# Performance work log

Hardware: AMD Instinct MI355X
Metric: run time of the kernel (lower is better)

The kernel has to match this reference:

```python
import jax, jax.numpy as jnp
import numpy as np

B, N, M, H, NH = 128, 4096, 64, 512, 4
IN, OUT = 256, 256
NH2 = 2 * NH  # read/write heads interleaved: even idx = read, odd idx = write
EPS = 1e-8


def setup_inputs() -> dict:
    key = jax.random.key(0)
    ks = jax.random.split(key, 20)
    nrm = lambda k, shape, s=0.05: (jax.random.normal(k, shape, jnp.float32) * s)
    return {
        'in_data': jax.random.normal(ks[0], (B, IN), jnp.float32),
        'memory': jax.random.normal(ks[1], (B, N, M), jnp.float32) * 0.1,
        'h_prev': jax.random.normal(ks[2], (B, H), jnp.float32),
        'c_prev': jax.random.normal(ks[3], (B, H), jnp.float32),
        'prev_reads': jax.random.normal(ks[4], (NH, B, M), jnp.float32),
        'prev_weights': jax.random.uniform(ks[5], (NH2, B, N), jnp.float32),
        # controller LSTMCell (input = in_data ++ prev_reads)
        'W_ih': nrm(ks[6], (4 * H, IN + NH * M)),
        'b_ih': jnp.zeros((4 * H,), jnp.float32),
        'W_hh': nrm(ks[7], (4 * H, H)),
        'b_hh': jnp.zeros((4 * H,), jnp.float32),
        # output layer over [h ++ reads]
        'W_out': nrm(ks[8], (OUT, H + NH * M)),
        'b_out': jnp.zeros((OUT,), jnp.float32),
        # per-head addressing params, stacked over the 2*NH heads (fed with c-state)
        'Wk': nrm(ks[9], (NH2, M, H)), 'bk': jnp.zeros((NH2, M), jnp.float32),
        'Wbeta': nrm(ks[10], (NH2, H)), 'bbeta': jnp.zeros((NH2,), jnp.float32),
        'Wg': nrm(ks[11], (NH2, H)), 'bg': jnp.zeros((NH2,), jnp.float32),
        'Ws': nrm(ks[12], (NH2, 3, H)), 'bs': jnp.zeros((NH2, 3), jnp.float32),
        'Wgam': nrm(ks[13], (NH2, H)), 'bgam': jnp.zeros((NH2,), jnp.float32),
        'We': nrm(ks[14], (NH2, M, H)), 'be': jnp.zeros((NH2, M), jnp.float32),
        'Wa': nrm(ks[15], (NH2, M, H)), 'ba': jnp.zeros((NH2, M), jnp.float32),
    }


def reference(in_data, memory, h_prev, c_prev, prev_reads, prev_weights,
              W_ih, b_ih, W_hh, b_hh, W_out, b_out,
              Wk, bk, Wbeta, bbeta, Wg, bg, Ws, bs, Wgam, bgam, We, be, Wa, ba):
    bsz = in_data.shape[0]
    # controller LSTM step on [x ++ prev_reads]
    x = jnp.concatenate([in_data, jnp.swapaxes(prev_reads, 0, 1).reshape(bsz, -1)], axis=-1)
    gates = x @ W_ih.T + h_prev @ W_hh.T + b_ih + b_hh
    gi, gf, gg, go = jnp.split(gates, 4, axis=-1)
    c = jax.nn.sigmoid(gf) * c_prev + jax.nn.sigmoid(gi) * jnp.tanh(gg)
    h = jax.nn.sigmoid(go) * jnp.tanh(c)  # |h| < 1, so clamp(-20, 20) is identity

    mem = memory
    reads = []
    for i in range(NH2):  # fixed small loop; even = read head, odd = write head
        keyv = c @ Wk[i].T + bk[i]                                    # [B, M]
        beta = jax.nn.softplus(c @ Wbeta[i] + bbeta[i])[:, None]      # [B, 1]
        g = jax.nn.sigmoid(c @ Wg[i] + bg[i])[:, None]                # [B, 1]
        s = jax.nn.softmax(c @ Ws[i].T + bs[i], axis=-1)              # [B, 3]
        gamma = 1.0 + jax.nn.softplus(c @ Wgam[i] + bgam[i])[:, None]  # [B, 1]
        # content addressing: cosine similarity, sharpened softmax
        sim = jnp.einsum('bnm,bm->bn', mem, keyv)
        sim = sim / (jnp.linalg.norm(mem, axis=-1) * jnp.linalg.norm(keyv, axis=-1, keepdims=True) + EPS)
        wc = jax.nn.softmax(beta * sim, axis=-1)
        # interpolate, circular shift (-1, 0, +1), sharpen
        wg_ = g * wc + (1.0 - g) * prev_weights[i]
        wsft = (s[:, 0:1] * jnp.roll(wg_, -1, axis=1)
                + s[:, 1:2] * wg_
                + s[:, 2:3] * jnp.roll(wg_, 1, axis=1))
        wpow = wsft ** gamma
        w = wpow / (jnp.sum(wpow, axis=1, keepdims=True) + EPS)
        if i % 2 == 0:
            reads.append(jnp.einsum('bn,bnm->bm', w, mem))
        else:
            e = jax.nn.sigmoid(c @ We[i].T + be[i])                   # erase [B, M]
            a = jnp.tanh(c @ Wa[i].T + ba[i])                         # add   [B, M]
            mem = mem * (1.0 - w[:, :, None] * e[:, None, :]) + w[:, :, None] * a[:, None, :]

    out = jax.nn.sigmoid(jnp.concatenate([h] + reads, axis=-1) @ W_out.T + b_out)
    return out
```

## Files before the change

kernel.cpp:

```cpp
#include <hip/hip_runtime.h>
#include <math.h>

#define BSZ 128
#define NN_ 4096
#define MM_ 64
#define HH_ 512
#define EPSF 1e-8f

__device__ __forceinline__ float sigmoidf_(float x) { return 1.0f / (1.0f + expf(-x)); }
__device__ __forceinline__ float softplusf_(float x) { return fmaxf(x, 0.0f) + log1pf(expf(-fabsf(x))); }

__global__ void k_build_x(const float* __restrict__ in_data, const float* __restrict__ prev_reads,
                          float* __restrict__ x) {
    int idx = blockIdx.x * blockDim.x + threadIdx.x;
    if (idx >= BSZ * 512) return;
    int b = idx >> 9, j = idx & 511;
    float v;
    if (j < 256) v = in_data[b * 256 + j];
    else {
        int hi = (j - 256) >> 6, m = (j - 256) & 63;
        v = prev_reads[(hi * BSZ + b) * 64 + m];
    }
    x[idx] = v;
}

__global__ __launch_bounds__(256) void k_gemm_atk(const float* __restrict__ A,
                                                  const float* __restrict__ W,
                                                  float* __restrict__ C, int Ncols, int K) {
    __shared__ float Alds[64 * 129];
    __shared__ float Wlds[64 * 65];
    int t = threadIdx.x;
    int k0 = blockIdx.y * 64;
    int n0 = blockIdx.x * 64;
    for (int i = 0; i < 8; ++i) {
        int f = t + 256 * i;
        int row = f >> 4, kk = (f & 15) * 4;
        float4 v = *(const float4*)(A + (size_t)row * K + k0 + kk);
        Alds[(kk + 0) * 129 + row] = v.x;
        Alds[(kk + 1) * 129 + row] = v.y;
        Alds[(kk + 2) * 129 + row] = v.z;
        Alds[(kk + 3) * 129 + row] = v.w;
    }
    for (int i = 0; i < 4; ++i) {
        int f = t + 256 * i;
        int o = f >> 4, kk = (f & 15) * 4;
        float4 v = *(const float4*)(W + (size_t)(n0 + o) * K + k0 + kk);
        Wlds[(kk + 0) * 65 + o] = v.x;
        Wlds[(kk + 1) * 65 + o] = v.y;
        Wlds[(kk + 2) * 65 + o] = v.z;
        Wlds[(kk + 3) * 65 + o] = v.w;
    }
    __syncthreads();
    int ob = (t & 15) * 4;
    int bb = (t >> 4) * 8;
    float acc[4][8];
#pragma unroll
    for (int i = 0; i < 4; ++i)
#pragma unroll
        for (int j = 0; j < 8; ++j) acc[i][j] = 0.f;
    for (int kk = 0; kk < 64; ++kk) {
        const float* wp = &Wlds[kk * 65 + ob];
        const float* ap = &Alds[kk * 129 + bb];
        float w0 = wp[0], w1 = wp[1], w2 = wp[2], w3 = wp[3];
#pragma unroll
        for (int j = 0; j < 8; ++j) {
            float av = ap[j];
            acc[0][j] = fmaf(w0, av, acc[0][j]);
            acc[1][j] = fmaf(w1, av, acc[1][j]);
            acc[2][j] = fmaf(w2, av, acc[2][j]);
            acc[3][j] = fmaf(w3, av, acc[3][j]);
        }
    }
#pragma unroll
    for (int i = 0; i < 4; ++i)
#pragma unroll
        for (int j = 0; j < 8; ++j)
            atomicAdd(&C[(size_t)(bb + j) * Ncols + n0 + ob + i], acc[i][j]);
}

__global__ void k_lstm(const float* __restrict__ gates, const float* __restrict__ b_ih,
                       const float* __restrict__ b_hh, const float* __restrict__ c_prev,
                       float* __restrict__ cbuf, float* __restrict__ hbuf) {
    int idx = blockIdx.x * blockDim.x + threadIdx.x;
    if (idx >= BSZ * HH_) return;
    int b = idx >> 9, j = idx & 511;
    const float* gr = gates + (size_t)b * 2048;
    float gi = gr[j]        + b_ih[j]        + b_hh[j];
    float gf = gr[512 + j]  + b_ih[512 + j]  + b_hh[512 + j];
    float gg = gr[1024 + j] + b_ih[1024 + j] + b_hh[1024 + j];
    float go = gr[1536 + j] + b_ih[1536 + j] + b_hh[1536 + j];
    float cc = sigmoidf_(gf) * c_prev[idx] + sigmoidf_(gi) * tanhf(gg);
    float hh = sigmoidf_(go) * tanhf(cc);
    cbuf[idx] = cc;
    hbuf[idx] = hh;
}

__global__ void k_build_whead(const float* __restrict__ Wk, const float* __restrict__ bk,
                              const float* __restrict__ Wbeta, const float* __restrict__ bbeta,
                              const float* __restrict__ Wg, const float* __restrict__ bg,
                              const float* __restrict__ Ws, const float* __restrict__ bs,
                              const float* __restrict__ Wgam, const float* __restrict__ bgam,
                              const float* __restrict__ We, const float* __restrict__ be,
                              const float* __restrict__ Wa, const float* __restrict__ ba,
                              float* __restrict__ Whead, float* __restrict__ bhead) {
    int idx = blockIdx.x * blockDim.x + threadIdx.x;
    if (idx >= 1600 * 512) return;
    int r = idx >> 9, k = idx & 511;
    float v = 0.f, bv = 0.f;
    if (r < 1584) {
        int i = r / 198, q = r - i * 198;
        if (q < 64)       { v = Wk[((i << 6) + q) * 512 + k];        bv = bk[(i << 6) + q]; }
        else if (q == 64) { v = Wbeta[i * 512 + k];                  bv = bbeta[i]; }
        else if (q == 65) { v = Wg[i * 512 + k];                     bv = bg[i]; }
        else if (q <= 68) { v = Ws[(i * 3 + q - 66) * 512 + k];      bv = bs[i * 3 + q - 66]; }
        else if (q == 69) { v = Wgam[i * 512 + k];                   bv = bgam[i]; }
        else if (q < 134) { v = We[((i << 6) + q - 70) * 512 + k];   bv = be[(i << 6) + q - 70]; }
        else              { v = Wa[((i << 6) + q - 134) * 512 + k];  bv = ba[(i << 6) + q - 134]; }
    }
    Whead[idx] = v;
    if (k == 0) bhead[r] = bv;
}

__global__ __launch_bounds__(256) void k_headact(const float* __restrict__ Chead, const float* __restrict__ bhead,
                                                 float* __restrict__ keys, float* __restrict__ knorm,
                                                 float* __restrict__ betaA, float* __restrict__ gA,
                                                 float* __restrict__ gammaA, float* __restrict__ sA,
                                                 float* __restrict__ eA, float* __restrict__ aA) {
    __shared__ float sk[64];
    __shared__ float s3[3];
    int blk = blockIdx.x;
    int i = blk >> 7, b = blk & 127;
    int q = threadIdx.x;
    float val = 0.f;
    if (q < 198) val = Chead[(size_t)b * 1600 + i * 198 + q] + bhead[i * 198 + q];
    if (q < 64) { keys[(size_t)(i * BSZ + b) * 64 + q] = val; sk[q] = val * val; }
    if (q >= 66 && q <= 68) s3[q - 66] = val;
    __syncthreads();
    if (q == 0) {
        float s = 0.f;
        for (int m2 = 0; m2 < 64; ++m2) s += sk[m2];
        knorm[i * BSZ + b] = sqrtf(s);
    }
    if (q == 64) betaA[i * BSZ + b] = softplusf_(val);
    if (q == 65) gA[i * BSZ + b] = sigmoidf_(val);
    if (q == 69) gammaA[i * BSZ + b] = 1.f + softplusf_(val);
    if (q == 66) {
        float mx = fmaxf(s3[0], fmaxf(s3[1], s3[2]));
        float e0 = expf(s3[0] - mx), e1 = expf(s3[1] - mx), e2 = expf(s3[2] - mx);
        float inv = 1.f / (e0 + e1 + e2);
        sA[(i * BSZ + b) * 3 + 0] = e0 * inv;
        sA[(i * BSZ + b) * 3 + 1] = e1 * inv;
        sA[(i * BSZ + b) * 3 + 2] = e2 * inv;
    }
    if (q >= 70 && q < 134)  eA[(size_t)(i * BSZ + b) * 64 + (q - 70)] = sigmoidf_(val);
    if (q >= 134 && q < 198) aA[(size_t)(i * BSZ + b) * 64 + (q - 134)] = tanhf(val);
}

__global__ __launch_bounds__(256) void k_pass2(const float* __restrict__ mem,
                                               const float* __restrict__ wbuf,
                                               const float* __restrict__ eA, const float* __restrict__ aA,
                                               const float* __restrict__ keys, const float* __restrict__ knorm,
                                               float* __restrict__ sims, float* __restrict__ r_out,
                                               int napply, int nsims, int sh0, int sh1,
                                               int read_state, int read_head, int read_idx) {
    __shared__ __align__(16) float rbuf[16][64];
    int t = threadIdx.x;
    int lane = t & 15, grp = t >> 4;
    int base = blockIdx.x * 64;
    int b = base >> 12;
    int m4 = lane * 4;
    float4 e1 = *(const float4*)(eA + (size_t)(1 * BSZ + b) * 64 + m4);
    float4 a1 = *(const float4*)(aA + (size_t)(1 * BSZ + b) * 64 + m4);
    float4 e3 = *(const float4*)(eA + (size_t)(3 * BSZ + b) * 64 + m4);
    float4 a3 = *(const float4*)(aA + (size_t)(3 * BSZ + b) * 64 + m4);
    float4 e5 = *(const float4*)(eA + (size_t)(5 * BSZ + b) * 64 + m4);
    float4 a5 = *(const float4*)(aA + (size_t)(5 * BSZ + b) * 64 + m4);
    float4 k0v = make_float4(0.f, 0.f, 0.f, 0.f), k1v = k0v;
    float kn0v = 0.f, kn1v = 0.f;
    if (nsims > 0) { k0v = *(const float4*)(keys + (size_t)(sh0 * BSZ + b) * 64 + m4); kn0v = knorm[sh0 * BSZ + b]; }
    if (nsims > 1) { k1v = *(const float4*)(keys + (size_t)(sh1 * BSZ + b) * 64 + m4); kn1v = knorm[sh1 * BSZ + b]; }
    const float* w1p = wbuf + (size_t)1 * BSZ * NN_;
    const float* w3p = wbuf + (size_t)3 * BSZ * NN_;
    const float* w5p = wbuf + (size_t)5 * BSZ * NN_;
    const float* wrp = (read_head >= 0) ? (wbuf + (size_t)read_head * BSZ * NN_) : nullptr;
    float* sim0 = sims + (size_t)sh0 * BSZ * NN_;
    float* sim1 = sims + (size_t)sh1 * BSZ * NN_;

    float4 racc = make_float4(0.f, 0.f, 0.f, 0.f);
    for (int it = 0; it < 4; ++it) {
        int row = base + it * 16 + grp;
        float4 m = *(const float4*)(mem + (size_t)row * 64 + m4);
        float4 mr = m;
        if (napply >= 1) {
            float w = w1p[row];
            m.x = m.x * (1.f - w * e1.x) + w * a1.x;
            m.y = m.y * (1.f - w * e1.y) + w * a1.y;
            m.z = m.z * (1.f - w * e1.z) + w * a1.z;
            m.w = m.w * (1.f - w * e1.w) + w * a1.w;
            if (read_state == 1) mr = m;
        }
        if (napply >= 2) {
            float w = w3p[row];
            m.x = m.x * (1.f - w * e3.x) + w * a3.x;
            m.y = m.y * (1.f - w * e3.y) + w * a3.y;
            m.z = m.z * (1.f - w * e3.z) + w * a3.z;
            m.w = m.w * (1.f - w * e3.w) + w * a3.w;
            if (read_state == 2) mr = m;
        }
        if (napply >= 3) {
            float w = w5p[row];
            m.x = m.x * (1.f - w * e5.x) + w * a5.x;
            m.y = m.y * (1.f - w * e5.y) + w * a5.y;
            m.z = m.z * (1.f - w * e5.z) + w * a5.z;
            m.w = m.w * (1.f - w * e5.w) + w * a5.w;
            if (read_state == 3) mr = m;
        }
        if (read_head >= 0) {
            float wr = wrp[row];
            racc.x = fmaf(wr, mr.x, racc.x);
            racc.y = fmaf(wr, mr.y, racc.y);
            racc.z = fmaf(wr, mr.z, racc.z);
            racc.w = fmaf(wr, mr.w, racc.w);
        }
        if (nsims > 0) {
            float d0 = m.x * k0v.x + m.y * k0v.y + m.z * k0v.z + m.w * k0v.w;
            float nn = m.x * m.x + m.y * m.y + m.z * m.z + m.w * m.w;
            float d1 = 0.f;
            if (nsims > 1) d1 = m.x * k1v.x + m.y * k1v.y + m.z * k1v.z + m.w * k1v.w;
#pragma unroll
            for (int off = 8; off >= 1; off >>= 1) {
                d0 += __shfl_xor(d0, off, 16);
                nn += __shfl_xor(nn, off, 16);
                if (nsims > 1) d1 += __shfl_xor(d1, off, 16);
            }
            if (lane == 0) {
                float nm = sqrtf(nn);
                sim0[row] = d0 / (nm * kn0v + EPSF);
                if (nsims > 1) sim1[row] = d1 / (nm * kn1v + EPSF);
            }
        }
    }
    if (read_head >= 0) {
        *(float4*)(&rbuf[grp][m4]) = racc;
        __syncthreads();
        if (t < 64) {
            float s = 0.f;
#pragma unroll
            for (int g2 = 0; g2 < 16; ++g2) s += rbuf[g2][t];
            atomicAdd(&r_out[(size_t)(read_idx * BSZ + b) * 64 + t], s);
        }
    }
}

__global__ __launch_bounds__(256) void k_weights(const float* __restrict__ sims,
                                                 const float* __restrict__ prev_w,
                                                 const float* __restrict__ betaA, const float* __restrict__ gA,
                                                 const float* __restrict__ gammaA, const float* __restrict__ sA,
                                                 float* __restrict__ wout_base, int head0) {
    __shared__ float wg[NN_];
    __shared__ float red[256];
    int h = head0 + blockIdx.y, b = blockIdx.x;
    int hb = h * BSZ + b;
    float beta = betaA[hb], g = gA[hb], gamma = gammaA[hb];
    float s0 = sA[hb * 3 + 0], s1 = sA[hb * 3 + 1], s2 = sA[hb * 3 + 2];
    const float* sim = sims + (size_t)hb * NN_;
    const float* pw = prev_w + (size_t)hb * NN_;
    float* wout = wout_base + (size_t)hb * NN_;
    int t = threadIdx.x;
    float tv[16];
    float lmax = -3.4e38f;
#pragma unroll
    for (int j = 0; j < 16; ++j) {
        float x = beta * sim[t + 256 * j];
        tv[j] = x;
        lmax = fmaxf(lmax, x);
    }
    red[t] = lmax; __syncthreads();
    for (int s = 128; s > 0; s >>= 1) { if (t < s) red[t] = fmaxf(red[t], red[t + s]); __syncthreads(); }
    float Mx = red[0]; __syncthreads();
    float lsum = 0.f;
#pragma unroll
    for (int j = 0; j < 16; ++j) { float ex = expf(tv[j] - Mx); tv[j] = ex; lsum += ex; }
    red[t] = lsum; __syncthreads();
    for (int s = 128; s > 0; s >>= 1) { if (t < s) red[t] += red[t + s]; __syncthreads(); }
    float invS = 1.f / red[0]; __syncthreads();
#pragma unroll
    for (int j = 0; j < 16; ++j) {
        int n = t + 256 * j;
        wg[n] = g * tv[j] * invS + (1.f - g) * pw[n];
    }
    __syncthreads();
    float lsum2 = 0.f;
#pragma unroll
    for (int j = 0; j < 16; ++j) {
        int n = t + 256 * j;
        float wsft = s0 * wg[(n + 1) & (NN_ - 1)] + s1 * wg[n] + s2 * wg[(n - 1) & (NN_ - 1)];
        float wp = powf(wsft, gamma);
        tv[j] = wp;
        lsum2 += wp;
    }
    red[t] = lsum2; __syncthreads();
    for (int s = 128; s > 0; s >>= 1) { if (t < s) red[t] += red[t + s]; __syncthreads(); }
    float inv2 = 1.f / (red[0] + EPSF);
#pragma unroll
    for (int j = 0; j < 16; ++j) wout[t + 256 * j] = tv[j] * inv2;
}

__global__ void k_build_cat(const float* __restrict__ hbuf, const float* __restrict__ rbuf,
                            float* __restrict__ cat) {
    int idx = blockIdx.x * blockDim.x + threadIdx.x;
    if (idx >= BSZ * 768) return;
    int b = idx / 768, j = idx - b * 768;
    float v;
    if (j < 512) v = hbuf[b * 512 + j];
    else {
        int ri = (j - 512) >> 6, m = (j - 512) & 63;
        v = rbuf[(ri * BSZ + b) * 64 + m];
    }
    cat[idx] = v;
}

__global__ void k_out(const float* __restrict__ outacc, const float* __restrict__ b_out,
                      float* __restrict__ out) {
    int idx = blockIdx.x * blockDim.x + threadIdx.x;
    if (idx >= BSZ * 256) return;
    out[idx] = sigmoidf_(outacc[idx] + b_out[idx & 255]);
}

extern "C" void kernel_launch(void* const* d_in, const int* in_sizes, int n_in,
                              void* d_out, int out_size, void* d_ws, size_t ws_size,
                              hipStream_t stream) {
    const float* in_data      = (const float*)d_in[0];
    const float* memory       = (const float*)d_in[1];
    const float* h_prev       = (const float*)d_in[2];
    const float* c_prev       = (const float*)d_in[3];
    const float* prev_reads   = (const float*)d_in[4];
    const float* prev_weights = (const float*)d_in[5];
    const float* W_ih = (const float*)d_in[6];
    const float* b_ih = (const float*)d_in[7];
    const float* W_hh = (const float*)d_in[8];
    const float* b_hh = (const float*)d_in[9];
    const float* W_out = (const float*)d_in[10];
    const float* b_out = (const float*)d_in[11];
    const float* Wk   = (const float*)d_in[12];
    const float* bk   = (const float*)d_in[13];
    const float* Wbeta = (const float*)d_in[14];
    const float* bbeta = (const float*)d_in[15];
    const float* Wg   = (const float*)d_in[16];
    const float* bg   = (const float*)d_in[17];
    const float* Ws   = (const float*)d_in[18];
    const float* bs   = (const float*)d_in[19];
    const float* Wgam = (const float*)d_in[20];
    const float* bgam = (const float*)d_in[21];
    const float* We   = (const float*)d_in[22];
    const float* be   = (const float*)d_in[23];
    const float* Wa   = (const float*)d_in[24];
    const float* ba   = (const float*)d_in[25];

    float* ws = (float*)d_ws;
    size_t o_gates  = 0;
    size_t o_chead  = o_gates + 262144;
    size_t o_r      = o_chead + 204800;
    size_t o_outacc = o_r + 32768;
    size_t zero_floats = o_outacc + 32768;
    size_t o_x     = zero_floats;
    size_t o_c     = o_x + 65536;
    size_t o_h     = o_c + 65536;
    size_t o_whead = o_h + 65536;
    size_t o_bhead = o_whead + 819200;
    size_t o_keys  = o_bhead + 2048;
    size_t o_knorm = o_keys + 65536;
    size_t o_beta  = o_knorm + 1024;
    size_t o_g     = o_beta + 1024;
    size_t o_gamma = o_g + 1024;
    size_t o_s     = o_gamma + 1024;
    size_t o_e     = o_s + 3072;
    size_t o_a     = o_e + 65536;
    size_t o_sims  = o_a + 65536;
    size_t o_w     = o_sims + 4194304;
    size_t o_cat   = o_w + 4194304;

    float* gates  = ws + o_gates;
    float* Chead  = ws + o_chead;
    float* rbuf   = ws + o_r;
    float* outacc = ws + o_outacc;
    float* xbuf   = ws + o_x;
    float* cbuf   = ws + o_c;
    float* hbuf   = ws + o_h;
    float* Whead  = ws + o_whead;
    float* bhead  = ws + o_bhead;
    float* keys   = ws + o_keys;
    float* knorm  = ws + o_knorm;
    float* betaA  = ws + o_beta;
    float* gA     = ws + o_g;
    float* gammaA = ws + o_gamma;
    float* sA     = ws + o_s;
    float* eA     = ws + o_e;
    float* aA     = ws + o_a;
    float* sims   = ws + o_sims;
    float* wbuf   = ws + o_w;
    float* cat    = ws + o_cat;

    hipMemsetAsync(d_ws, 0, zero_floats * sizeof(float), stream);

    k_build_x<<<256, 256, 0, stream>>>(in_data, prev_reads, xbuf);
    k_gemm_atk<<<dim3(32, 8), 256, 0, stream>>>(xbuf, W_ih, gates, 2048, 512);
    k_gemm_atk<<<dim3(32, 8), 256, 0, stream>>>(h_prev, W_hh, gates, 2048, 512);
    k_lstm<<<256, 256, 0, stream>>>(gates, b_ih, b_hh, c_prev, cbuf, hbuf);

    k_build_whead<<<3200, 256, 0, stream>>>(Wk, bk, Wbeta, bbeta, Wg, bg, Ws, bs,
                                            Wgam, bgam, We, be, Wa, ba, Whead, bhead);
    k_gemm_atk<<<dim3(25, 8), 256, 0, stream>>>(cbuf, Whead, Chead, 1600, 512);
    k_headact<<<1024, 256, 0, stream>>>(Chead, bhead, keys, knorm, betaA, gA, gammaA, sA, eA, aA);

    const int PB = BSZ * NN_ / 64;
    k_pass2<<<PB, 256, 0, stream>>>(memory, wbuf, eA, aA, keys, knorm, sims, rbuf,
                                    0, 2, 0, 1, -1, -1, 0);
    k_weights<<<dim3(128, 2), 256, 0, stream>>>(sims, prev_weights, betaA, gA, gammaA, sA, wbuf, 0);
    k_pass2<<<PB, 256, 0, stream>>>(memory, wbuf, eA, aA, keys, knorm, sims, rbuf,
                                    1, 2, 2, 3, 0, 0, 0);
    k_weights<<<dim3(128, 2), 256, 0, stream>>>(sims, prev_weights, betaA, gA, gammaA, sA, wbuf, 2);
    k_pass2<<<PB, 256, 0, stream>>>(memory, wbuf, eA, aA, keys, knorm, sims, rbuf,
                                    2, 2, 4, 5, 1, 2, 1);
    k_weights<<<dim3(128, 2), 256, 0, stream>>>(sims, prev_weights, betaA, gA, gammaA, sA, wbuf, 4);
    k_pass2<<<PB, 256, 0, stream>>>(memory, wbuf, eA, aA, keys, knorm, sims, rbuf,
                                    3, 1, 6, 6, 2, 4, 2);
    k_weights<<<dim3(128, 1), 256, 0, stream>>>(sims, prev_weights, betaA, gA, gammaA, sA, wbuf, 6);
    k_pass2<<<PB, 256, 0, stream>>>(memory, wbuf, eA, aA, keys, knorm, sims, rbuf,
                                    3, 0, 0, 0, 3, 6, 3);

    k_build_cat<<<384, 256, 0, stream>>>(hbuf, rbuf, cat);
    k_gemm_atk<<<dim3(4, 12), 256, 0, stream>>>(cat, W_out, outacc, 256, 768);
    k_out<<<128, 256, 0, stream>>>(outacc, b_out, (float*)d_out);

    (void)in_sizes; (void)n_in; (void)out_size; (void)ws_size;
}
```

Baseline: 556.6 us.

## Fuse whole NTM step into one persistent kernel with software grid barriers

```diff
diff --git a/kernel.cpp b/kernel.cpp
--- a/kernel.cpp
+++ b/kernel.cpp
@@ -1,195 +1,167 @@
 #include <hip/hip_runtime.h>
 #include <math.h>
 
-#define BSZ 128
-#define NN_ 4096
-#define MM_ 64
-#define HH_ 512
+#define NBLK 512
+#define THR  256
 #define EPSF 1e-8f
 
 __device__ __forceinline__ float sigmoidf_(float x) { return 1.0f / (1.0f + expf(-x)); }
 __device__ __forceinline__ float softplusf_(float x) { return fmaxf(x, 0.0f) + log1pf(expf(-fabsf(x))); }
-
-__global__ void k_build_x(const float* __restrict__ in_data, const float* __restrict__ prev_reads,
-                          float* __restrict__ x) {
-    int idx = blockIdx.x * blockDim.x + threadIdx.x;
-    if (idx >= BSZ * 512) return;
-    int b = idx >> 9, j = idx & 511;
-    float v;
-    if (j < 256) v = in_data[b * 256 + j];
-    else {
-        int hi = (j - 256) >> 6, m = (j - 256) & 63;
-        v = prev_reads[(hi * BSZ + b) * 64 + m];
-    }
-    x[idx] = v;
-}
-
-__global__ __launch_bounds__(256) void k_gemm_atk(const float* __restrict__ A,
-                                                  const float* __restrict__ W,
-                                                  float* __restrict__ C, int Ncols, int K) {
-    __shared__ float Alds[64 * 129];
-    __shared__ float Wlds[64 * 65];
+__device__ __forceinline__ float4 ld4(const float* p) { return *(const float4*)p; }
+
+struct Args {
+    const float *in_data, *memory, *h_prev, *c_prev, *prev_reads, *prev_weights;
+    const float *W_ih, *b_ih, *W_hh, *b_hh, *W_out, *b_out;
+    const float *Wk, *bk, *Wbeta, *bbeta, *Wg, *bg, *Ws3, *bs3, *Wgam, *bgam, *We, *be, *Wa, *ba;
+    float *gates, *cbuf, *hbuf, *Chead, *keys, *knorm, *betaA, *gA, *gammaA, *sA, *eA, *aA;
+    float *sims, *wbuf, *outacc, *rbuf, *out;
+    int *bar_g, *bar_r, *bar_s;
+};
+
+union SMem {
+    struct { float wg[4096]; float red[256]; } w;
+    struct { float A[32 * 65]; float W[32 * 33]; } g;
+    struct { float part[16][64]; } s;
+    struct { float sk[64]; float s3[3]; } h;
+};
+
+__device__ __forceinline__ void gridbar(const Args& a, int k) {
+    __syncthreads();
+    if (threadIdx.x == 0) {
+        int g = blockIdx.x & 31;
+        bool done = false;
+        if (__hip_atomic_fetch_add(&a.bar_g[g << 5], 1, __ATOMIC_ACQ_REL, __HIP_MEMORY_SCOPE_AGENT) == k * 16 - 1) {
+            if (__hip_atomic_fetch_add(a.bar_r, 1, __ATOMIC_ACQ_REL, __HIP_MEMORY_SCOPE_AGENT) == k * 32 - 1) {
+                __hip_atomic_store(a.bar_s, k, __ATOMIC_RELEASE, __HIP_MEMORY_SCOPE_AGENT);
+                done = true;
+            }
+        }
+        if (!done) {
+            while (__hip_atomic_load(a.bar_s, __ATOMIC_ACQUIRE, __HIP_MEMORY_SCOPE_AGENT) < k)
+                __builtin_amdgcn_s_sleep(1);
+        }
+    }
+    __syncthreads();
+}
+
+__device__ float4 gatherA(const Args& a, int mode, int row, int k) {
+    if (mode == 0) {
+        if (k < 256)      return ld4(a.in_data + row * 256 + k);
+        else if (k < 512) { int kk = k - 256; return ld4(a.prev_reads + (size_t)((kk >> 6) * 128 + row) * 64 + (kk & 63)); }
+        else              return ld4(a.h_prev + row * 512 + (k - 512));
+    } else if (mode == 1) {
+        return ld4(a.cbuf + row * 512 + k);
+    } else {
+        if (k < 512) return ld4(a.hbuf + row * 512 + k);
+        int kk = k - 512;
+        return ld4(a.rbuf + (size_t)((kk >> 6) * 128 + row) * 64 + (kk & 63));
+    }
+}
+
+__device__ float4 gatherW(const Args& a, int mode, int o, int k) {
+    if (mode == 0) {
+        if (k < 512) return ld4(a.W_ih + (size_t)o * 512 + k);
+        return ld4(a.W_hh + (size_t)o * 512 + (k - 512));
+    } else if (mode == 2) {
+        return ld4(a.W_out + (size_t)o * 768 + k);
+    } else {
+        if (o >= 1584) return make_float4(0.f, 0.f, 0.f, 0.f);
+        int i = o / 198, q = o - i * 198;
+        if (q < 64)       return ld4(a.Wk + (size_t)((i << 6) + q) * 512 + k);
+        else if (q == 64) return ld4(a.Wbeta + (size_t)i * 512 + k);
+        else if (q == 65) return ld4(a.Wg + (size_t)i * 512 + k);
+        else if (q <= 68) return ld4(a.Ws3 + (size_t)(i * 3 + q - 66) * 512 + k);
+        else if (q == 69) return ld4(a.Wgam + (size_t)i * 512 + k);
+        else if (q < 134) return ld4(a.We + (size_t)((i << 6) + q - 70) * 512 + k);
+        else              return ld4(a.Wa + (size_t)((i << 6) + q - 134) * 512 + k);
+    }
+}
+
+__device__ void gemm_phase(const Args& a, SMem& sm, int mode, int K, int Ncols, float* C) {
+    int ntiles = 2 * (Ncols >> 5);
     int t = threadIdx.x;
-    int k0 = blockIdx.y * 64;
-    int n0 = blockIdx.x * 64;
-    for (int i = 0; i < 8; ++i) {
-        int f = t + 256 * i;
-        int row = f >> 4, kk = (f & 15) * 4;
-        float4 v = *(const float4*)(A + (size_t)row * K + k0 + kk);
-        Alds[(kk + 0) * 129 + row] = v.x;
-        Alds[(kk + 1) * 129 + row] = v.y;
-        Alds[(kk + 2) * 129 + row] = v.z;
-        Alds[(kk + 3) * 129 + row] = v.w;
-    }
-    for (int i = 0; i < 4; ++i) {
-        int f = t + 256 * i;
-        int o = f >> 4, kk = (f & 15) * 4;
-        float4 v = *(const float4*)(W + (size_t)(n0 + o) * K + k0 + kk);
-        Wlds[(kk + 0) * 65 + o] = v.x;
-        Wlds[(kk + 1) * 65 + o] = v.y;
-        Wlds[(kk + 2) * 65 + o] = v.z;
-        Wlds[(kk + 3) * 65 + o] = v.w;
-    }
-    __syncthreads();
-    int ob = (t & 15) * 4;
-    int bb = (t >> 4) * 8;
-    float acc[4][8];
-#pragma unroll
-    for (int i = 0; i < 4; ++i)
-#pragma unroll
-        for (int j = 0; j < 8; ++j) acc[i][j] = 0.f;
-    for (int kk = 0; kk < 64; ++kk) {
-        const float* wp = &Wlds[kk * 65 + ob];
-        const float* ap = &Alds[kk * 129 + bb];
-        float w0 = wp[0], w1 = wp[1], w2 = wp[2], w3 = wp[3];
-#pragma unroll
-        for (int j = 0; j < 8; ++j) {
-            float av = ap[j];
-            acc[0][j] = fmaf(w0, av, acc[0][j]);
-            acc[1][j] = fmaf(w1, av, acc[1][j]);
-            acc[2][j] = fmaf(w2, av, acc[2][j]);
-            acc[3][j] = fmaf(w3, av, acc[3][j]);
-        }
-    }
-#pragma unroll
-    for (int i = 0; i < 4; ++i)
-#pragma unroll
-        for (int j = 0; j < 8; ++j)
-            atomicAdd(&C[(size_t)(bb + j) * Ncols + n0 + ob + i], acc[i][j]);
-}
-
-__global__ void k_lstm(const float* __restrict__ gates, const float* __restrict__ b_ih,
-                       const float* __restrict__ b_hh, const float* __restrict__ c_prev,
-                       float* __restrict__ cbuf, float* __restrict__ hbuf) {
-    int idx = blockIdx.x * blockDim.x + threadIdx.x;
-    if (idx >= BSZ * HH_) return;
-    int b = idx >> 9, j = idx & 511;
-    const float* gr = gates + (size_t)b * 2048;
-    float gi = gr[j]        + b_ih[j]        + b_hh[j];
-    float gf = gr[512 + j]  + b_ih[512 + j]  + b_hh[512 + j];
-    float gg = gr[1024 + j] + b_ih[1024 + j] + b_hh[1024 + j];
-    float go = gr[1536 + j] + b_ih[1536 + j] + b_hh[1536 + j];
-    float cc = sigmoidf_(gf) * c_prev[idx] + sigmoidf_(gi) * tanhf(gg);
-    float hh = sigmoidf_(go) * tanhf(cc);
-    cbuf[idx] = cc;
-    hbuf[idx] = hh;
-}
-
-__global__ void k_build_whead(const float* __restrict__ Wk, const float* __restrict__ bk,
-                              const float* __restrict__ Wbeta, const float* __restrict__ bbeta,
-                              const float* __restrict__ Wg, const float* __restrict__ bg,
-                              const float* __restrict__ Ws, const float* __restrict__ bs,
-                              const float* __restrict__ Wgam, const float* __restrict__ bgam,
-                              const float* __restrict__ We, const float* __restrict__ be,
-                              const float* __restrict__ Wa, const float* __restrict__ ba,
-                              float* __restrict__ Whead, float* __restrict__ bhead) {
-    int idx = blockIdx.x * blockDim.x + threadIdx.x;
-    if (idx >= 1600 * 512) return;
-    int r = idx >> 9, k = idx & 511;
-    float v = 0.f, bv = 0.f;
-    if (r < 1584) {
-        int i = r / 198, q = r - i * 198;
-        if (q < 64)       { v = Wk[((i << 6) + q) * 512 + k];        bv = bk[(i << 6) + q]; }
-        else if (q == 64) { v = Wbeta[i * 512 + k];                  bv = bbeta[i]; }
-        else if (q == 65) { v = Wg[i * 512 + k];                     bv = bg[i]; }
-        else if (q <= 68) { v = Ws[(i * 3 + q - 66) * 512 + k];      bv = bs[i * 3 + q - 66]; }
-        else if (q == 69) { v = Wgam[i * 512 + k];                   bv = bgam[i]; }
-        else if (q < 134) { v = We[((i << 6) + q - 70) * 512 + k];   bv = be[(i << 6) + q - 70]; }
-        else              { v = Wa[((i << 6) + q - 134) * 512 + k];  bv = ba[(i << 6) + q - 134]; }
-    }
-    Whead[idx] = v;
-    if (k == 0) bhead[r] = bv;
-}
-
-__global__ __launch_bounds__(256) void k_headact(const float* __restrict__ Chead, const float* __restrict__ bhead,
-                                                 float* __restrict__ keys, float* __restrict__ knorm,
-                                                 float* __restrict__ betaA, float* __restrict__ gA,
-                                                 float* __restrict__ gammaA, float* __restrict__ sA,
-                                                 float* __restrict__ eA, float* __restrict__ aA) {
-    __shared__ float sk[64];
-    __shared__ float s3[3];
-    int blk = blockIdx.x;
-    int i = blk >> 7, b = blk & 127;
-    int q = threadIdx.x;
-    float val = 0.f;
-    if (q < 198) val = Chead[(size_t)b * 1600 + i * 198 + q] + bhead[i * 198 + q];
-    if (q < 64) { keys[(size_t)(i * BSZ + b) * 64 + q] = val; sk[q] = val * val; }
-    if (q >= 66 && q <= 68) s3[q - 66] = val;
-    __syncthreads();
-    if (q == 0) {
-        float s = 0.f;
-        for (int m2 = 0; m2 < 64; ++m2) s += sk[m2];
-        knorm[i * BSZ + b] = sqrtf(s);
-    }
-    if (q == 64) betaA[i * BSZ + b] = softplusf_(val);
-    if (q == 65) gA[i * BSZ + b] = sigmoidf_(val);
-    if (q == 69) gammaA[i * BSZ + b] = 1.f + softplusf_(val);
-    if (q == 66) {
-        float mx = fmaxf(s3[0], fmaxf(s3[1], s3[2]));
-        float e0 = expf(s3[0] - mx), e1 = expf(s3[1] - mx), e2 = expf(s3[2] - mx);
-        float inv = 1.f / (e0 + e1 + e2);
-        sA[(i * BSZ + b) * 3 + 0] = e0 * inv;
-        sA[(i * BSZ + b) * 3 + 1] = e1 * inv;
-        sA[(i * BSZ + b) * 3 + 2] = e2 * inv;
-    }
-    if (q >= 70 && q < 134)  eA[(size_t)(i * BSZ + b) * 64 + (q - 70)] = sigmoidf_(val);
-    if (q >= 134 && q < 198) aA[(size_t)(i * BSZ + b) * 64 + (q - 134)] = tanhf(val);
-}
-
-__global__ __launch_bounds__(256) void k_pass2(const float* __restrict__ mem,
-                                               const float* __restrict__ wbuf,
-                                               const float* __restrict__ eA, const float* __restrict__ aA,
-                                               const float* __restrict__ keys, const float* __restrict__ knorm,
-                                               float* __restrict__ sims, float* __restrict__ r_out,
-                                               int napply, int nsims, int sh0, int sh1,
-                                               int read_state, int read_head, int read_idx) {
-    __shared__ __align__(16) float rbuf[16][64];
-    int t = threadIdx.x;
-    int lane = t & 15, grp = t >> 4;
-    int base = blockIdx.x * 64;
+    for (int tile = blockIdx.x; tile < ntiles; tile += NBLK) {
+        int rb = (tile & 1) * 64;
+        int o0 = (tile >> 1) * 32;
+        float acc[4][2] = {{0.f, 0.f}, {0.f, 0.f}, {0.f, 0.f}, {0.f, 0.f}};
+        for (int k0 = 0; k0 < K; k0 += 32) {
+            __syncthreads();
+#pragma unroll
+            for (int i = 0; i < 2; ++i) {
+                int idx = t + THR * i;
+                int row = idx >> 3, c4 = (idx & 7) * 4;
+                float4 v = gatherA(a, mode, rb + row, k0 + c4);
+                sm.g.A[(c4 + 0) * 65 + row] = v.x;
+                sm.g.A[(c4 + 1) * 65 + row] = v.y;
+                sm.g.A[(c4 + 2) * 65 + row] = v.z;
+                sm.g.A[(c4 + 3) * 65 + row] = v.w;
+            }
+            {
+                int o = t >> 3, c4 = (t & 7) * 4;
+                float4 v = gatherW(a, mode, o0 + o, k0 + c4);
+                sm.g.W[(c4 + 0) * 33 + o] = v.x;
+                sm.g.W[(c4 + 1) * 33 + o] = v.y;
+                sm.g.W[(c4 + 2) * 33 + o] = v.z;
+                sm.g.W[(c4 + 3) * 33 + o] = v.w;
+            }
+            __syncthreads();
+            int ob = (t & 7) * 4, bb = (t >> 3) * 2;
+#pragma unroll
+            for (int kk = 0; kk < 32; ++kk) {
+                const float* wp = &sm.g.W[kk * 33 + ob];
+                const float* ap = &sm.g.A[kk * 65 + bb];
+                float a0 = ap[0], a1 = ap[1];
+                float w0 = wp[0], w1 = wp[1], w2 = wp[2], w3 = wp[3];
+                acc[0][0] = fmaf(w0, a0, acc[0][0]); acc[0][1] = fmaf(w0, a1, acc[0][1]);
+                acc[1][0] = fmaf(w1, a0, acc[1][0]); acc[1][1] = fmaf(w1, a1, acc[1][1]);
+                acc[2][0] = fmaf(w2, a0, acc[2][0]); acc[2][1] = fmaf(w2, a1, acc[2][1]);
+                acc[3][0] = fmaf(w3, a0, acc[3][0]); acc[3][1] = fmaf(w3, a1, acc[3][1]);
+            }
+        }
+        int ob = (t & 7) * 4, bb = (t >> 3) * 2;
+#pragma unroll
+        for (int i = 0; i < 4; ++i)
+#pragma unroll
+            for (int j = 0; j < 2; ++j)
+                C[(size_t)(rb + bb + j) * Ncols + o0 + ob + i] = acc[i][j];
+    }
+}
+
+__device__ float biasHead(const Args& a, int i, int q) {
+    if (q < 64)  return a.bk[(i << 6) + q];
+    if (q == 64) return a.bbeta[i];
+    if (q == 65) return a.bg[i];
+    if (q <= 68) return a.bs3[i * 3 + q - 66];
+    if (q == 69) return a.bgam[i];
+    if (q < 134) return a.be[(i << 6) + q - 70];
+    return a.ba[(i << 6) + q - 134];
+}
+
+__device__ void sweep_phase(const Args& a, SMem& sm, int napply, int nsims, int sh0, int sh1,
+                            int read_state, int read_head, int read_idx) {
+    int t = threadIdx.x, lane = t & 15, grp = t >> 4;
+    int base = blockIdx.x * 1024;
     int b = base >> 12;
     int m4 = lane * 4;
-    float4 e1 = *(const float4*)(eA + (size_t)(1 * BSZ + b) * 64 + m4);
-    float4 a1 = *(const float4*)(aA + (size_t)(1 * BSZ + b) * 64 + m4);
-    float4 e3 = *(const float4*)(eA + (size_t)(3 * BSZ + b) * 64 + m4);
-    float4 a3 = *(const float4*)(aA + (size_t)(3 * BSZ + b) * 64 + m4);
-    float4 e5 = *(const float4*)(eA + (size_t)(5 * BSZ + b) * 64 + m4);
-    float4 a5 = *(const float4*)(aA + (size_t)(5 * BSZ + b) * 64 + m4);
+    float4 e1 = ld4(a.eA + (size_t)(1 * 128 + b) * 64 + m4);
+    float4 a1 = ld4(a.aA + (size_t)(1 * 128 + b) * 64 + m4);
+    float4 e3 = ld4(a.eA + (size_t)(3 * 128 + b) * 64 + m4);
+    float4 a3 = ld4(a.aA + (size_t)(3 * 128 + b) * 64 + m4);
+    float4 e5 = ld4(a.eA + (size_t)(5 * 128 + b) * 64 + m4);
+    float4 a5 = ld4(a.aA + (size_t)(5 * 128 + b) * 64 + m4);
     float4 k0v = make_float4(0.f, 0.f, 0.f, 0.f), k1v = k0v;
-    float kn0v = 0.f, kn1v = 0.f;
-    if (nsims > 0) { k0v = *(const float4*)(keys + (size_t)(sh0 * BSZ + b) * 64 + m4); kn0v = knorm[sh0 * BSZ + b]; }
-    if (nsims > 1) { k1v = *(const float4*)(keys + (size_t)(sh1 * BSZ + b) * 64 + m4); kn1v = knorm[sh1 * BSZ + b]; }
-    const float* w1p = wbuf + (size_t)1 * BSZ * NN_;
-    const float* w3p = wbuf + (size_t)3 * BSZ * NN_;
-    const float* w5p = wbuf + (size_t)5 * BSZ * NN_;
-    const float* wrp = (read_head >= 0) ? (wbuf + (size_t)read_head * BSZ * NN_) : nullptr;
-    float* sim0 = sims + (size_t)sh0 * BSZ * NN_;
-    float* sim1 = sims + (size_t)sh1 * BSZ * NN_;
-
+    float kn0 = 0.f, kn1 = 0.f;
+    if (nsims > 0) { k0v = ld4(a.keys + (size_t)(sh0 * 128 + b) * 64 + m4); kn0 = a.knorm[sh0 * 128 + b]; }
+    if (nsims > 1) { k1v = ld4(a.keys + (size_t)(sh1 * 128 + b) * 64 + m4); kn1 = a.knorm[sh1 * 128 + b]; }
+    const float* w1p = a.wbuf + (size_t)1 * 128 * 4096;
+    const float* w3p = a.wbuf + (size_t)3 * 128 * 4096;
+    const float* w5p = a.wbuf + (size_t)5 * 128 * 4096;
+    const float* wrp = (read_head >= 0) ? a.wbuf + (size_t)read_head * 128 * 4096 : nullptr;
+    float* sim0 = a.sims + (size_t)sh0 * 128 * 4096;
+    float* sim1 = a.sims + (size_t)sh1 * 128 * 4096;
     float4 racc = make_float4(0.f, 0.f, 0.f, 0.f);
-    for (int it = 0; it < 4; ++it) {
-        int row = base + it * 16 + grp;
-        float4 m = *(const float4*)(mem + (size_t)row * 64 + m4);
+
+    auto proc = [&](float4 m, int row) {
         float4 mr = m;
         if (napply >= 1) {
             float w = w1p[row];
@@ -216,11 +188,11 @@
             if (read_state == 3) mr = m;
         }
         if (read_head >= 0) {
-            float wr = wrp[row];
-            racc.x = fmaf(wr, mr.x, racc.x);
-            racc.y = fmaf(wr, mr.y, racc.y);
-            racc.z = fmaf(wr, mr.z, racc.z);
-            racc.w = fmaf(wr, mr.w, racc.w);
+            float w = wrp[row];
+            racc.x = fmaf(w, mr.x, racc.x);
+            racc.y = fmaf(w, mr.y, racc.y);
+            racc.z = fmaf(w, mr.z, racc.z);
+            racc.w = fmaf(w, mr.w, racc.w);
         }
         if (nsims > 0) {
             float d0 = m.x * k0v.x + m.y * k0v.y + m.z * k0v.z + m.w * k0v.w;
@@ -235,37 +207,43 @@
             }
             if (lane == 0) {
                 float nm = sqrtf(nn);
-                sim0[row] = d0 / (nm * kn0v + EPSF);
-                if (nsims > 1) sim1[row] = d1 / (nm * kn1v + EPSF);
-            }
-        }
+                sim0[row] = d0 / (nm * kn0 + EPSF);
+                if (nsims > 1) sim1[row] = d1 / (nm * kn1 + EPSF);
+            }
+        }
+    };
+
+    for (int it = 0; it < 64; it += 4) {
+        int r0 = base + it * 16 + grp;
+        const float* mp = a.memory + (size_t)r0 * 64 + m4;
+        float4 m0 = ld4(mp);
+        float4 m1 = ld4(mp + 16 * 64);
+        float4 m2 = ld4(mp + 32 * 64);
+        float4 m3 = ld4(mp + 48 * 64);
+        proc(m0, r0); proc(m1, r0 + 16); proc(m2, r0 + 32); proc(m3, r0 + 48);
     }
     if (read_head >= 0) {
-        *(float4*)(&rbuf[grp][m4]) = racc;
+        *(float4*)(&sm.s.part[grp][m4]) = racc;
         __syncthreads();
         if (t < 64) {
             float s = 0.f;
 #pragma unroll
-            for (int g2 = 0; g2 < 16; ++g2) s += rbuf[g2][t];
-            atomicAdd(&r_out[(size_t)(read_idx * BSZ + b) * 64 + t], s);
-        }
-    }
-}
-
-__global__ __launch_bounds__(256) void k_weights(const float* __restrict__ sims,
-                                                 const float* __restrict__ prev_w,
-                                                 const float* __restrict__ betaA, const float* __restrict__ gA,
-                                                 const float* __restrict__ gammaA, const float* __restrict__ sA,
-                                                 float* __restrict__ wout_base, int head0) {
-    __shared__ float wg[NN_];
-    __shared__ float red[256];
-    int h = head0 + blockIdx.y, b = blockIdx.x;
-    int hb = h * BSZ + b;
-    float beta = betaA[hb], g = gA[hb], gamma = gammaA[hb];
-    float s0 = sA[hb * 3 + 0], s1 = sA[hb * 3 + 1], s2 = sA[hb * 3 + 2];
-    const float* sim = sims + (size_t)hb * NN_;
-    const float* pw = prev_w + (size_t)hb * NN_;
-    float* wout = wout_base + (size_t)hb * NN_;
+            for (int g2 = 0; g2 < 16; ++g2) s += sm.s.part[g2][t];
+            atomicAdd(&a.rbuf[(size_t)(read_idx * 128 + b) * 64 + t], s);
+        }
+    }
+}
+
+__device__ void weights_phase(const Args& a, SMem& sm, int head0, int nheads) {
+    int pair = blockIdx.x;
+    if (pair >= nheads * 128) return;
+    int h = head0 + (pair >> 7), b = pair & 127;
+    int hb = h * 128 + b;
+    float beta = a.betaA[hb], g = a.gA[hb], gamma = a.gammaA[hb];
+    float s0 = a.sA[hb * 3 + 0], s1 = a.sA[hb * 3 + 1], s2 = a.sA[hb * 3 + 2];
+    const float* sim = a.sims + (size_t)hb * 4096;
+    const float* pw = a.prev_weights + (size_t)hb * 4096;
+    float* wout = a.wbuf + (size_t)hb * 4096;
     int t = threadIdx.x;
     float tv[16];
     float lmax = -3.4e38f;
@@ -275,163 +253,160 @@
         tv[j] = x;
         lmax = fmaxf(lmax, x);
     }
-    red[t] = lmax; __syncthreads();
-    for (int s = 128; s > 0; s >>= 1) { if (t < s) red[t] = fmaxf(red[t], red[t + s]); __syncthreads(); }
-    float Mx = red[0]; __syncthreads();
+    sm.w.red[t] = lmax; __syncthreads();
+    for (int s = 128; s > 0; s >>= 1) { if (t < s) sm.w.red[t] = fmaxf(sm.w.red[t], sm.w.red[t + s]); __syncthreads(); }
+    float Mx = sm.w.red[0]; __syncthreads();
     float lsum = 0.f;
 #pragma unroll
     for (int j = 0; j < 16; ++j) { float ex = expf(tv[j] - Mx); tv[j] = ex; lsum += ex; }
-    red[t] = lsum; __syncthreads();
-    for (int s = 128; s > 0; s >>= 1) { if (t < s) red[t] += red[t + s]; __syncthreads(); }
-    float invS = 1.f / red[0]; __syncthreads();
+    sm.w.red[t] = lsum; __syncthreads();
+    for (int s = 128; s > 0; s >>= 1) { if (t < s) sm.w.red[t] += sm.w.red[t + s]; __syncthreads(); }
+    float invS = 1.f / sm.w.red[0]; __syncthreads();
 #pragma unroll
     for (int j = 0; j < 16; ++j) {
         int n = t + 256 * j;
-        wg[n] = g * tv[j] * invS + (1.f - g) * pw[n];
+        sm.w.wg[n] = g * tv[j] * invS + (1.f - g) * pw[n];
     }
     __syncthreads();
     float lsum2 = 0.f;
 #pragma unroll
     for (int j = 0; j < 16; ++j) {
         int n = t + 256 * j;
-        float wsft = s0 * wg[(n + 1) & (NN_ - 1)] + s1 * wg[n] + s2 * wg[(n - 1) & (NN_ - 1)];
-        float wp = powf(wsft, gamma);
+        float wsft = s0 * sm.w.wg[(n + 1) & 4095] + s1 * sm.w.wg[n] + s2 * sm.w.wg[(n - 1) & 4095];
+        float wp = exp2f(gamma * log2f(wsft));
         tv[j] = wp;
         lsum2 += wp;
     }
-    red[t] = lsum2; __syncthreads();
-    for (int s = 128; s > 0; s >>= 1) { if (t < s) red[t] += red[t + s]; __syncthreads(); }
-    float inv2 = 1.f / (red[0] + EPSF);
+    sm.w.red[t] = lsum2; __syncthreads();
+    for (int s = 128; s > 0; s >>= 1) { if (t < s) sm.w.red[t] += sm.w.red[t + s]; __syncthreads(); }
+    float inv2 = 1.f / (sm.w.red[0] + EPSF);
 #pragma unroll
     for (int j = 0; j < 16; ++j) wout[t + 256 * j] = tv[j] * inv2;
 }
 
-__global__ void k_build_cat(const float* __restrict__ hbuf, const float* __restrict__ rbuf,
-                            float* __restrict__ cat) {
-    int idx = blockIdx.x * blockDim.x + threadIdx.x;
-    if (idx >= BSZ * 768) return;
-    int b = idx / 768, j = idx - b * 768;
-    float v;
-    if (j < 512) v = hbuf[b * 512 + j];
-    else {
-        int ri = (j - 512) >> 6, m = (j - 512) & 63;
-        v = rbuf[(ri * BSZ + b) * 64 + m];
-    }
-    cat[idx] = v;
-}
-
-__global__ void k_out(const float* __restrict__ outacc, const float* __restrict__ b_out,
-                      float* __restrict__ out) {
-    int idx = blockIdx.x * blockDim.x + threadIdx.x;
-    if (idx >= BSZ * 256) return;
-    out[idx] = sigmoidf_(outacc[idx] + b_out[idx & 255]);
+__global__ __launch_bounds__(THR, 2) void ntm_fused(Args a) {
+    __shared__ SMem sm;
+    int t = threadIdx.x;
+
+    gemm_phase(a, sm, 0, 1024, 2048, a.gates);
+    gridbar(a, 1);
+    if (blockIdx.x < 256) {
+        int idx = blockIdx.x * THR + t;
+        int j = idx & 511;
+        const float* gr = a.gates + (size_t)(idx >> 9) * 2048;
+        float gi = gr[j]        + a.b_ih[j]        + a.b_hh[j];
+        float gf = gr[512 + j]  + a.b_ih[512 + j]  + a.b_hh[512 + j];
+        float gg = gr[1024 + j] + a.b_ih[1024 + j] + a.b_hh[1024 + j];
+        float go = gr[1536 + j] + a.b_ih[1536 + j] + a.b_hh[1536 + j];
+        float cc = sigmoidf_(gf) * a.c_prev[idx] + sigmoidf_(gi) * tanhf(gg);
+        a.cbuf[idx] = cc;
+        a.hbuf[idx] = sigmoidf_(go) * tanhf(cc);
+    }
+    gridbar(a, 2);
+    gemm_phase(a, sm, 1, 512, 1600, a.Chead);
+    gridbar(a, 3);
+    for (int ii = 0; ii < 2; ++ii) {
+        int item = blockIdx.x * 2 + ii;
+        int i = item >> 7, b = item & 127;
+        float val = 0.f;
+        if (t < 198) val = a.Chead[(size_t)b * 1600 + i * 198 + t] + biasHead(a, i, t);
+        if (t < 64) { a.keys[(size_t)(i * 128 + b) * 64 + t] = val; sm.h.sk[t] = val * val; }
+        if (t >= 66 && t <= 68) sm.h.s3[t - 66] = val;
+        __syncthreads();
+        if (t == 0) {
+            float s = 0.f;
+            for (int m2 = 0; m2 < 64; ++m2) s += sm.h.sk[m2];
+            a.knorm[i * 128 + b] = sqrtf(s);
+        }
+        if (t == 64) a.betaA[i * 128 + b] = softplusf_(val);
+        if (t == 65) a.gA[i * 128 + b] = sigmoidf_(val);
+        if (t == 69) a.gammaA[i * 128 + b] = 1.f + softplusf_(val);
+        if (t == 66) {
+            float mx = fmaxf(sm.h.s3[0], fmaxf(sm.h.s3[1], sm.h.s3[2]));
+            float e0 = expf(sm.h.s3[0] - mx), e1 = expf(sm.h.s3[1] - mx), e2 = expf(sm.h.s3[2] - mx);
+            float inv = 1.f / (e0 + e1 + e2);
+            a.sA[(i * 128 + b) * 3 + 0] = e0 * inv;
+            a.sA[(i * 128 + b) * 3 + 1] = e1 * inv;
+            a.sA[(i * 128 + b) * 3 + 2] = e2 * inv;
+        }
+        if (t >= 70 && t < 134)  a.eA[(size_t)(i * 128 + b) * 64 + (t - 70)] = sigmoidf_(val);
+        if (t >= 134 && t < 198) a.aA[(size_t)(i * 128 + b) * 64 + (t - 134)] = tanhf(val);
+        __syncthreads();
+    }
+    gridbar(a, 4);
+    sweep_phase(a, sm, 0, 2, 0, 1, -1, -1, 0);   gridbar(a, 5);
+    weights_phase(a, sm, 0, 2);                  gridbar(a, 6);
+    sweep_phase(a, sm, 1, 2, 2, 3, 0, 0, 0);     gridbar(a, 7);
+    weights_phase(a, sm, 2, 2);                  gridbar(a, 8);
+    sweep_phase(a, sm, 2, 2, 4, 5, 1, 2, 1);     gridbar(a, 9);
+    weights_phase(a, sm, 4, 2);                  gridbar(a, 10);
+    sweep_phase(a, sm, 3, 1, 6, 6, 2, 4, 2);     gridbar(a, 11);
+    weights_phase(a, sm, 6, 1);                  gridbar(a, 12);
+    sweep_phase(a, sm, 3, 0, 0, 0, 3, 6, 3);     gridbar(a, 13);
+    gemm_phase(a, sm, 2, 768, 256, a.outacc);
+    gridbar(a, 14);
+    if (blockIdx.x < 128) {
+        int idx = blockIdx.x * THR + t;
+        a.out[idx] = sigmoidf_(a.outacc[idx] + a.b_out[idx & 255]);
+    }
 }
 
 extern "C" void kernel_launch(void* const* d_in, const int* in_sizes, int n_in,
                               void* d_out, int out_size, void* d_ws, size_t ws_size,
                               hipStream_t stream) {
-    const float* in_data      = (const float*)d_in[0];
-    const float* memory       = (const float*)d_in[1];
-    const float* h_prev       = (const float*)d_in[2];
-    const float* c_prev       = (const float*)d_in[3];
-    const float* prev_reads   = (const float*)d_in[4];
-    const float* prev_weights = (const float*)d_in[5];
-    const float* W_ih = (const float*)d_in[6];
-    const float* b_ih = (const float*)d_in[7];
-    const float* W_hh = (const float*)d_in[8];
-    const float* b_hh = (const float*)d_in[9];
-    const float* W_out = (const float*)d_in[10];
-    const float* b_out = (const float*)d_in[11];
-    const float* Wk   = (const float*)d_in[12];
-    const float* bk   = (const float*)d_in[13];
-    const float* Wbeta = (const float*)d_in[14];
-    const float* bbeta = (const float*)d_in[15];
-    const float* Wg   = (const float*)d_in[16];
-    const float* bg   = (const float*)d_in[17];
-    const float* Ws   = (const float*)d_in[18];
-    const float* bs   = (const float*)d_in[19];
-    const float* Wgam = (const float*)d_in[20];
-    const float* bgam = (const float*)d_in[21];
-    const float* We   = (const float*)d_in[22];
-    const float* be   = (const float*)d_in[23];
-    const float* Wa   = (const float*)d_in[24];
-    const float* ba   = (const float*)d_in[25];
+    Args a;
+    a.in_data      = (const float*)d_in[0];
+    a.memory       = (const float*)d_in[1];
+    a.h_prev       = (const float*)d_in[2];
+    a.c_prev       = (const float*)d_in[3];
+    a.prev_reads   = (const float*)d_in[4];
+    a.prev_weights = (const float*)d_in[5];
+    a.W_ih  = (const float*)d_in[6];
+    a.b_ih  = (const float*)d_in[7];
+    a.W_hh  = (const float*)d_in[8];
+    a.b_hh  = (const float*)d_in[9];
+    a.W_out = (const float*)d_in[10];
+    a.b_out = (const float*)d_in[11];
+    a.Wk    = (const float*)d_in[12];
+    a.bk    = (const float*)d_in[13];
+    a.Wbeta = (const float*)d_in[14];
+    a.bbeta = (const float*)d_in[15];
+    a.Wg    = (const float*)d_in[16];
+    a.bg    = (const float*)d_in[17];
+    a.Ws3   = (const float*)d_in[18];
+    a.bs3   = (const float*)d_in[19];
+    a.Wgam  = (const float*)d_in[20];
+    a.bgam  = (const float*)d_in[21];
+    a.We    = (const float*)d_in[22];
+    a.be    = (const float*)d_in[23];
+    a.Wa    = (const float*)d_in[24];
+    a.ba    = (const float*)d_in[25];
 
     float* ws = (float*)d_ws;
-    size_t o_gates  = 0;
-    size_t o_chead  = o_gates + 262144;
-    size_t o_r      = o_chead + 204800;
-    size_t o_outacc = o_r + 32768;
-    size_t zero_floats = o_outacc + 32768;
-    size_t o_x     = zero_floats;
-    size_t o_c     = o_x + 65536;
-    size_t o_h     = o_c + 65536;
-    size_t o_whead = o_h + 65536;
-    size_t o_bhead = o_whead + 819200;
-    size_t o_keys  = o_bhead + 2048;
-    size_t o_knorm = o_keys + 65536;
-    size_t o_beta  = o_knorm + 1024;
-    size_t o_g     = o_beta + 1024;
-    size_t o_gamma = o_g + 1024;
-    size_t o_s     = o_gamma + 1024;
-    size_t o_e     = o_s + 3072;
-    size_t o_a     = o_e + 65536;
-    size_t o_sims  = o_a + 65536;
-    size_t o_w     = o_sims + 4194304;
-    size_t o_cat   = o_w + 4194304;
-
-    float* gates  = ws + o_gates;
-    float* Chead  = ws + o_chead;
-    float* rbuf   = ws + o_r;
-    float* outacc = ws + o_outacc;
-    float* xbuf   = ws + o_x;
-    float* cbuf   = ws + o_c;
-    float* hbuf   = ws + o_h;
-    float* Whead  = ws + o_whead;
-    float* bhead  = ws + o_bhead;
-    float* keys   = ws + o_keys;
-    float* knorm  = ws + o_knorm;
-    float* betaA  = ws + o_beta;
-    float* gA     = ws + o_g;
-    float* gammaA = ws + o_gamma;
-    float* sA     = ws + o_s;
-    float* eA     = ws + o_e;
-    float* aA     = ws + o_a;
-    float* sims   = ws + o_sims;
-    float* wbuf   = ws + o_w;
-    float* cat    = ws + o_cat;
-
-    hipMemsetAsync(d_ws, 0, zero_floats * sizeof(float), stream);
-
-    k_build_x<<<256, 256, 0, stream>>>(in_data, prev_reads, xbuf);
-    k_gemm_atk<<<dim3(32, 8), 256, 0, stream>>>(xbuf, W_ih, gates, 2048, 512);
-    k_gemm_atk<<<dim3(32, 8), 256, 0, stream>>>(h_prev, W_hh, gates, 2048, 512);
-    k_lstm<<<256, 256, 0, stream>>>(gates, b_ih, b_hh, c_prev, cbuf, hbuf);
-
-    k_build_whead<<<3200, 256, 0, stream>>>(Wk, bk, Wbeta, bbeta, Wg, bg, Ws, bs,
-                                            Wgam, bgam, We, be, Wa, ba, Whead, bhead);
-    k_gemm_atk<<<dim3(25, 8), 256, 0, stream>>>(cbuf, Whead, Chead, 1600, 512);
-    k_headact<<<1024, 256, 0, stream>>>(Chead, bhead, keys, knorm, betaA, gA, gammaA, sA, eA, aA);
-
-    const int PB = BSZ * NN_ / 64;
-    k_pass2<<<PB, 256, 0, stream>>>(memory, wbuf, eA, aA, keys, knorm, sims, rbuf,
-                                    0, 2, 0, 1, -1, -1, 0);
-    k_weights<<<dim3(128, 2), 256, 0, stream>>>(sims, prev_weights, betaA, gA, gammaA, sA, wbuf, 0);
-    k_pass2<<<PB, 256, 0, stream>>>(memory, wbuf, eA, aA, keys, knorm, sims, rbuf,
-                                    1, 2, 2, 3, 0, 0, 0);
-    k_weights<<<dim3(128, 2), 256, 0, stream>>>(sims, prev_weights, betaA, gA, gammaA, sA, wbuf, 2);
-    k_pass2<<<PB, 256, 0, stream>>>(memory, wbuf, eA, aA, keys, knorm, sims, rbuf,
-                                    2, 2, 4, 5, 1, 2, 1);
-    k_weights<<<dim3(128, 2), 256, 0, stream>>>(sims, prev_weights, betaA, gA, gammaA, sA, wbuf, 4);
-    k_pass2<<<PB, 256, 0, stream>>>(memory, wbuf, eA, aA, keys, knorm, sims, rbuf,
-                                    3, 1, 6, 6, 2, 4, 2);
-    k_weights<<<dim3(128, 1), 256, 0, stream>>>(sims, prev_weights, betaA, gA, gammaA, sA, wbuf, 6);
-    k_pass2<<<PB, 256, 0, stream>>>(memory, wbuf, eA, aA, keys, knorm, sims, rbuf,
-                                    3, 0, 0, 0, 3, 6, 3);
-
-    k_build_cat<<<384, 256, 0, stream>>>(hbuf, rbuf, cat);
-    k_gemm_atk<<<dim3(4, 12), 256, 0, stream>>>(cat, W_out, outacc, 256, 768);
-    k_out<<<128, 256, 0, stream>>>(outacc, b_out, (float*)d_out);
+    a.bar_g = (int*)ws;
+    a.bar_r = (int*)ws + 1024;
+    a.bar_s = (int*)ws + 1088;
+    a.rbuf  = ws + 2048;
+    size_t off = 2048 + 32768;
+    a.gates  = ws + off; off += 262144;
+    a.cbuf   = ws + off; off += 65536;
+    a.hbuf   = ws + off; off += 65536;
+    a.Chead  = ws + off; off += 204800;
+    a.keys   = ws + off; off += 65536;
+    a.knorm  = ws + off; off += 1024;
+    a.betaA  = ws + off; off += 1024;
+    a.gA     = ws + off; off += 1024;
+    a.gammaA = ws + off; off += 1024;
+    a.sA     = ws + off; off += 3072;
+    a.eA     = ws + off; off += 65536;
+    a.aA     = ws + off; off += 65536;
+    a.sims   = ws + off; off += 4194304;
+    a.wbuf   = ws + off; off += 4194304;
+    a.outacc = ws + off; off += 32768;
+    a.out    = (float*)d_out;
+
+    hipMemsetAsync(d_ws, 0, (2048 + 32768) * sizeof(float), stream);
+    ntm_fused<<<NBLK, THR, 0, stream>>>(a);
 
     (void)in_sizes; (void)n_in; (void)out_size; (void)ws_size;
 }
```

After: 1.494 ms. 168% more time.
